# Optimization experiments

Measured on AMD Instinct MI355X. Metric: run time of the kernel, lower is better.

## Reference

```python
import jax, jax.numpy as jnp
import numpy as np

B, S, D = 16, 512, 384
MAX_DUR = 16  # durations drawn from [0, 16)


def setup_inputs() -> dict:
    key = jax.random.key(0)
    k1, k2 = jax.random.split(key)
    hidden = jax.random.normal(k1, (B, S, D), dtype=jnp.float32)
    durations = jax.random.randint(k2, (B, S), 0, MAX_DUR, dtype=jnp.int32)
    return {"hidden": hidden, "durations": durations}


def reference(hidden, durations):
    # hidden: [B, S, D], durations: [B, S] int
    out_lengths = durations.sum(axis=1)              # [B]
    # NOTE: output length is data-dependent (matches torch eager semantics);
    # concretize it here. Under jit one would pass a static max_length instead.
    max_length = int(out_lengths.max())
    csum = jnp.cumsum(durations, axis=1)             # [B, S] inclusive cumsum
    pos = jnp.arange(max_length)                     # [L]
    # Output frame j of batch b copies token t where csum[b,t-1] <= j < csum[b,t]
    # (tokens with duration 0 are skipped automatically by side='right').
    idx = jax.vmap(lambda c: jnp.searchsorted(c, pos, side='right'))(csum)  # [B, L]
    idx = jnp.minimum(idx, hidden.shape[1] - 1)      # clamp padding region
    out = jnp.take_along_axis(hidden, idx[:, :, None], axis=1)  # [B, L, D]
    # zero out positions beyond each batch's expanded length (torch init zeros)
    valid = (pos[None, :] < out_lengths[:, None]).astype(hidden.dtype)  # [B, L]
    out = out * valid[:, :, None]
    return out, out_lengths
```

## Files before the change

kernel.cpp:

```cpp
#include <hip/hip_runtime.h>

#define B_CONST 16
#define S_CONST 512
#define D_CONST 384

__global__ void scan_kernel(const int* __restrict__ dur, int* __restrict__ csum,
                            int* __restrict__ lenArr, float* __restrict__ outLenF) {
    int b = blockIdx.x;
    int s = threadIdx.x;
    int v = dur[b * S_CONST + s];
    int lane = s & 63;
    int wave = s >> 6;
    int x = v;
    #pragma unroll
    for (int off = 1; off < 64; off <<= 1) {
        int y = __shfl_up(x, off, 64);
        if (lane >= off) x += y;
    }
    __shared__ int wsum[8];
    if (lane == 63) wsum[wave] = x;
    __syncthreads();
    if (s == 0) {
        int acc = 0;
        #pragma unroll
        for (int w = 0; w < 8; ++w) { int t = wsum[w]; wsum[w] = acc; acc += t; }
    }
    __syncthreads();
    x += wsum[wave];
    csum[b * S_CONST + s] = x;
    if (s == S_CONST - 1) {
        lenArr[b] = x;
        outLenF[b] = (float)x;
    }
}

__global__ void idx_kernel(const int* __restrict__ csum, const int* __restrict__ lenArr,
                           int* __restrict__ gidx, int L) {
    int t = blockIdx.x * blockDim.x + threadIdx.x;
    if (t >= B_CONST * L) return;
    int b = t / L;
    int j = t - b * L;
    if (j >= lenArr[b]) { gidx[t] = -1; return; }
    const int* c = csum + b * S_CONST;
    int lo = 0, hi = S_CONST;
    while (lo < hi) {
        int mid = (lo + hi) >> 1;
        if (c[mid] <= j) lo = mid + 1; else hi = mid;
    }
    if (lo > S_CONST - 1) lo = S_CONST - 1;
    gidx[t] = b * S_CONST + lo;
}

__global__ void gather_kernel(const float4* __restrict__ hidden4,
                              const int* __restrict__ gidx,
                              float4* __restrict__ out4, int total4) {
    int t = blockIdx.x * blockDim.x + threadIdx.x;
    if (t >= total4) return;
    const int K = D_CONST / 4;
    int row = t / K;
    int k = t - row * K;
    int g = gidx[row];
    float4 val;
    if (g < 0) {
        val = make_float4(0.f, 0.f, 0.f, 0.f);
    } else {
        val = hidden4[(size_t)g * K + k];
    }
    out4[t] = val;
}

extern "C" void kernel_launch(void* const* d_in, const int* in_sizes, int n_in,
                              void* d_out, int out_size, void* d_ws, size_t ws_size,
                              hipStream_t stream) {
    const int* durations = (const int*)d_in[1];
    const float* hidden  = (const float*)d_in[0];
    float* out = (float*)d_out;

    int L = (out_size - B_CONST) / (B_CONST * D_CONST);

    int* csum   = (int*)d_ws;
    int* lenArr = csum + B_CONST * S_CONST;
    int* gidx   = lenArr + B_CONST;

    float* outLenF = out + (size_t)B_CONST * L * D_CONST;

    scan_kernel<<<B_CONST, S_CONST, 0, stream>>>(durations, csum, lenArr, outLenF);

    int nIdx = B_CONST * L;
    idx_kernel<<<(nIdx + 255) / 256, 256, 0, stream>>>(csum, lenArr, gidx, L);

    int total4 = B_CONST * L * (D_CONST / 4);
    gather_kernel<<<(total4 + 255) / 256, 256, 0, stream>>>(
        (const float4*)hidden, gidx, (float4*)out, total4);
}
```

Before: 128.9 us.

## Fuse scan, index search, and gather into one kernel with per-block redundant scan

Replaces the three launches (scan, index search, gather) with one kernel. Each block redundantly computes the batch's prefix sum in shared memory, binary-searches token indices for its 16 output rows, then copies those rows. This removes two launches and the global workspace round trips for csum and gidx. In exchange, every block repeats the 512-element scan and adds extra barriers.

Measured after the change: 118.8 us. 7.8% less time.

```diff
diff --git a/kernel.cpp b/kernel.cpp
--- a/kernel.cpp
+++ b/kernel.cpp
@@ -1,95 +1,96 @@
 #include <hip/hip_runtime.h>
 
-#define B_CONST 16
-#define S_CONST 512
-#define D_CONST 384
+#define NB 16
+#define NS 512
+#define ND 384
+#define K4 (ND/4)
+#define ROWS 16
+#define NT 256
 
-__global__ void scan_kernel(const int* __restrict__ dur, int* __restrict__ csum,
-                            int* __restrict__ lenArr, float* __restrict__ outLenF) {
-    int b = blockIdx.x;
-    int s = threadIdx.x;
-    int v = dur[b * S_CONST + s];
-    int lane = s & 63;
-    int wave = s >> 6;
-    int x = v;
+__global__ __launch_bounds__(NT) void length_regulator_fused(
+    const float4* __restrict__ hidden4,
+    const int*    __restrict__ dur,
+    float4*       __restrict__ out4,
+    float*        __restrict__ outLenF,
+    int L)
+{
+    const int t = threadIdx.x;
+    const int b = blockIdx.y;
+    const int chunk = blockIdx.x;
+    const int j0 = chunk * ROWS;
+
+    __shared__ int csum[NS];
+    __shared__ int wsum[NT / 64];
+    __shared__ int rowTok[ROWS];
+
+    int2 d2 = ((const int2*)(dur + b * NS))[t];
+    int local = d2.x + d2.y;
+    int lane = t & 63, wave = t >> 6;
+    int x = local;
     #pragma unroll
     for (int off = 1; off < 64; off <<= 1) {
         int y = __shfl_up(x, off, 64);
         if (lane >= off) x += y;
     }
-    __shared__ int wsum[8];
     if (lane == 63) wsum[wave] = x;
     __syncthreads();
-    if (s == 0) {
+    if (t == 0) {
         int acc = 0;
         #pragma unroll
-        for (int w = 0; w < 8; ++w) { int t = wsum[w]; wsum[w] = acc; acc += t; }
+        for (int w = 0; w < NT / 64; ++w) { int tmp = wsum[w]; wsum[w] = acc; acc += tmp; }
     }
     __syncthreads();
-    x += wsum[wave];
-    csum[b * S_CONST + s] = x;
-    if (s == S_CONST - 1) {
-        lenArr[b] = x;
-        outLenF[b] = (float)x;
+    int excl = wsum[wave] + x - local;
+    csum[2 * t]     = excl + d2.x;
+    csum[2 * t + 1] = excl + local;
+    __syncthreads();
+
+    const int total = csum[NS - 1];
+
+    if (chunk == 0 && t == 0) outLenF[b] = (float)total;
+
+    if (t < ROWS) {
+        int j = j0 + t;
+        int g = -1;
+        if (j < L && j < total) {
+            int lo = 0, hi = NS;
+            while (lo < hi) {
+                int mid = (lo + hi) >> 1;
+                if (csum[mid] <= j) lo = mid + 1; else hi = mid;
+            }
+            if (lo > NS - 1) lo = NS - 1;
+            g = lo;
+        }
+        rowTok[t] = g;
     }
-}
+    __syncthreads();
 
-__global__ void idx_kernel(const int* __restrict__ csum, const int* __restrict__ lenArr,
-                           int* __restrict__ gidx, int L) {
-    int t = blockIdx.x * blockDim.x + threadIdx.x;
-    if (t >= B_CONST * L) return;
-    int b = t / L;
-    int j = t - b * L;
-    if (j >= lenArr[b]) { gidx[t] = -1; return; }
-    const int* c = csum + b * S_CONST;
-    int lo = 0, hi = S_CONST;
-    while (lo < hi) {
-        int mid = (lo + hi) >> 1;
-        if (c[mid] <= j) lo = mid + 1; else hi = mid;
+    const size_t outBase = ((size_t)b * L + j0) * K4;
+    #pragma unroll
+    for (int i = t; i < ROWS * K4; i += NT) {
+        int r = i / K4;
+        int k = i - r * K4;
+        int j = j0 + r;
+        if (j >= L) break;
+        int g = rowTok[r];
+        float4 v;
+        if (g < 0) v = make_float4(0.f, 0.f, 0.f, 0.f);
+        else       v = hidden4[(size_t)(b * NS + g) * K4 + k];
+        out4[outBase + i] = v;
     }
-    if (lo > S_CONST - 1) lo = S_CONST - 1;
-    gidx[t] = b * S_CONST + lo;
-}
-
-__global__ void gather_kernel(const float4* __restrict__ hidden4,
-                              const int* __restrict__ gidx,
-                              float4* __restrict__ out4, int total4) {
-    int t = blockIdx.x * blockDim.x + threadIdx.x;
-    if (t >= total4) return;
-    const int K = D_CONST / 4;
-    int row = t / K;
-    int k = t - row * K;
-    int g = gidx[row];
-    float4 val;
-    if (g < 0) {
-        val = make_float4(0.f, 0.f, 0.f, 0.f);
-    } else {
-        val = hidden4[(size_t)g * K + k];
-    }
-    out4[t] = val;
 }
 
 extern "C" void kernel_launch(void* const* d_in, const int* in_sizes, int n_in,
                               void* d_out, int out_size, void* d_ws, size_t ws_size,
                               hipStream_t stream) {
-    const int* durations = (const int*)d_in[1];
-    const float* hidden  = (const float*)d_in[0];
+    const float* hidden   = (const float*)d_in[0];
+    const int*   durations = (const int*)d_in[1];
     float* out = (float*)d_out;
 
-    int L = (out_size - B_CONST) / (B_CONST * D_CONST);
+    int L = (out_size - NB) / (NB * ND);
+    float* outLenF = out + (size_t)NB * L * ND;
 
-    int* csum   = (int*)d_ws;
-    int* lenArr = csum + B_CONST * S_CONST;
-    int* gidx   = lenArr + B_CONST;
-
-    float* outLenF = out + (size_t)B_CONST * L * D_CONST;
-
-    scan_kernel<<<B_CONST, S_CONST, 0, stream>>>(durations, csum, lenArr, outLenF);
-
-    int nIdx = B_CONST * L;
-    idx_kernel<<<(nIdx + 255) / 256, 256, 0, stream>>>(csum, lenArr, gidx, L);
-
-    int total4 = B_CONST * L * (D_CONST / 4);
-    gather_kernel<<<(total4 + 255) / 256, 256, 0, stream>>>(
-        (const float4*)hidden, gidx, (float4*)out, total4);
+    dim3 grid((L + ROWS - 1) / ROWS, NB);
+    length_regulator_fused<<<grid, NT, 0, stream>>>(
+        (const float4*)hidden, durations, (float4*)out, outLenF, L);
 }
```
